# Performance work log

Measured on AMD Instinct MI355X. Metric: run time of the kernel, lower is better.

The kernel has to match this reference:

```python
import jax, jax.numpy as jnp
import numpy as np

PATCH = 16
ATT_DEPTH = 2
DOWN = 2 ** ATT_DEPTH  # 4


def _unfold(x, p):
    # torch nn.Unfold(kernel=p, stride=p) on (B, C, H, W) single-channel slices,
    # vectorized over C. Returns (B, C, p*p, L) with L = (H//p)*(W//p),
    # kernel elements in row-major order, patches in row-major order (matches torch).
    B, C, H, W = x.shape
    xr = x.reshape(B, C, H // p, p, W // p, p)
    xr = xr.transpose(0, 1, 3, 5, 2, 4)  # (B, C, p, p, H//p, W//p)
    return xr.reshape(B, C, p * p, (H // p) * (W // p))


def setup_inputs() -> dict:
    key = jax.random.key(0)
    k1, k2, k3 = jax.random.split(key, 3)
    B, C, H, W = 8, 4, 1024, 1024
    L = (H // PATCH) * (W // PATCH)            # 4096
    L2 = (H // DOWN // PATCH) * (W // DOWN // PATCH)  # 256
    pred = jax.random.normal(k1, (B, C, H, W), dtype=jnp.float32)
    target = jax.random.randint(k2, (B, H, W), 0, C, dtype=jnp.int64)
    attentions = jax.random.uniform(k3, (B, C, L, L2), dtype=jnp.float32)
    return {"pred": pred, "target": target, "attentions": attentions}


def reference(pred, target, attentions):
    B, C, H, W = pred.shape
    # activation (softmax over class dim); pred is not used further in the loss,
    # kept for faithfulness to the original forward.
    _ = jax.nn.softmax(pred, axis=1)
    # one-hot ground truth, (B, C, H, W) float32
    y_gt = (target[:, None, :, :] == jnp.arange(C, dtype=target.dtype)[None, :, None, None]).astype(jnp.float32)
    # grouped conv with all-ones 4x4 kernel, stride 4, divided by 16 == 4x4 average pool
    y_gt_conv = y_gt.reshape(B, C, H // DOWN, DOWN, W // DOWN, DOWN).mean(axis=(3, 5))
    # unfold both maps: (B, C, p*p, L) and (B, C, p*p, L2)
    u_gt = _unfold(y_gt, PATCH)
    u_conv = _unfold(y_gt_conv, PATCH)
    # att[b,c,l,m] = sum_k u_gt[b,c,k,l] * u_conv[b,c,k,m] / p^2
    attentions_gt = jnp.einsum('bckl,bckm->bclm', u_gt, u_conv) / float(PATCH * PATCH)
    # MSE (mean reduction)
    return jnp.mean((attentions - attentions_gt) ** 2)
```

## Files before the change

kernel.cpp:

```cpp
#include <hip/hip_runtime.h>
#include <stdint.h>


#define BDIM 256

typedef int v4i  __attribute__((ext_vector_type(4)));
typedef int v16i __attribute__((ext_vector_type(16)));

__global__ __launch_bounds__(BDIM) void prep_kernel(
    const int* __restrict__ tgt, uint8_t* __restrict__ cls,
    uint8_t* __restrict__ cntT, float* __restrict__ dout) {
  __shared__ uint4 lcls[16][17];
  const int t   = threadIdx.x;
  const int blk = blockIdx.x;
  if (blk == 0 && t == 0) *dout = 0.f;
  const int b  = blk >> 8;
  const int hr = (blk >> 2) & 63;
  const int wq = blk & 3;

  {
    const int row = t >> 4, wb = t & 15;
    const int* p = tgt + ((size_t)b << 20) + ((size_t)((hr << 4) + row) << 10)
                 + (wq << 8) + (wb << 4);
    uint32_t o[4];
#pragma unroll
    for (int i = 0; i < 4; ++i) {
      int4 v = *(const int4*)(p + (i << 2));
      o[i] = (uint32_t)v.x | ((uint32_t)v.y << 8) |
             ((uint32_t)v.z << 16) | ((uint32_t)v.w << 24);
    }
    lcls[row][wb] = make_uint4(o[0], o[1], o[2], o[3]);
  }
  __syncthreads();

  {
    const int wb = t >> 4, ky = t & 15;
    const int l = (hr << 6) + (wq << 4) + wb;
    *(uint4*)(cls + ((size_t)b << 20) + ((size_t)l << 8) + (ky << 4)) =
        lcls[ky][wb];
  }

  {
    const int py = t >> 6, px = t & 63;
    uint32_t pc = 0;
#pragma unroll
    for (int dy = 0; dy < 4; ++dy) {
      uint32_t wv = ((const uint32_t*)&lcls[(py << 2) + dy][px >> 2])[px & 3];
#pragma unroll
      for (int s = 0; s < 32; s += 8)
        pc += 1u << (((wv >> s) & 3u) << 3);
    }
    const int Y = (hr << 2) + py, X = (wq << 6) + px;
    const int m  = ((Y >> 4) << 4) | (X >> 4);
    const int km = ((Y & 15) << 4) | (X & 15);
    size_t o = ((size_t)b << 18) | ((size_t)m << 8) | (size_t)km;
#pragma unroll
    for (int c = 0; c < 4; ++c)
      cntT[o + ((size_t)c << 16)] = (uint8_t)((pc >> (c << 3)) & 0xFFu);
  }
}

__global__ __launch_bounds__(BDIM) void gemm_kernel(
    const uint8_t* __restrict__ cls, const uint8_t* __restrict__ cntT,
    const float* __restrict__ att, float* __restrict__ dout) {
  __shared__ float wsum[4];
  const int t    = threadIdx.x;
  const int wv   = t >> 6, lane = t & 63;
  const int bc   = blockIdx.y;
  const int b    = bc >> 2, c = bc & 3;
  const int l0   = (blockIdx.x << 7) + (wv << 5);
  const int lrow  = lane & 31;
  const int khalf = lane >> 5;

  const uint32_t crep = (uint32_t)c * 0x01010101u;
  v4i afr[8];
  const uint8_t* abase = cls + ((size_t)b << 20) +
                         ((size_t)(l0 + lrow) << 8) + (khalf << 4);
#pragma unroll
  for (int kk = 0; kk < 8; ++kk) {
    uint4 raw = *(const uint4*)(abase + (kk << 5));
    uint32_t r[4] = {raw.x, raw.y, raw.z, raw.w};
    v4i a;
#pragma unroll
    for (int i = 0; i < 4; ++i) {
      uint32_t x = r[i] ^ crep;
      uint32_t nz = (x | (x >> 1)) & 0x01010101u;
      a[i] = (int)(nz ^ 0x01010101u);
    }
    afr[kk] = a;
  }

  const uint8_t* bbase = cntT + ((size_t)bc << 16) + (khalf << 4);
  const float* attbase = att + ((size_t)bc << 20) +
                         ((size_t)(l0 + (khalf << 2)) << 8) + lrow;
  float lsum = 0.f;

#pragma unroll 1
  for (int mc = 0; mc < 8; ++mc) {
    const float* ap = attbase + (mc << 5);
    float av[16];
#pragma unroll
    for (int reg = 0; reg < 16; ++reg)
      av[reg] = ap[((reg & 3) << 8) + ((reg >> 2) << 11)];

    v16i acc = {0,0,0,0,0,0,0,0,0,0,0,0,0,0,0,0};
    const uint8_t* bb = bbase + ((size_t)((mc << 5) + lrow) << 8);
#pragma unroll
    for (int kk = 0; kk < 8; ++kk) {
      uint4 raw = *(const uint4*)(bb + (kk << 5));
      v4i bfr;
      bfr[0] = (int)raw.x; bfr[1] = (int)raw.y;
      bfr[2] = (int)raw.z; bfr[3] = (int)raw.w;
      acc = __builtin_amdgcn_mfma_i32_32x32x32_i8(afr[kk], bfr, acc, 0, 0, 0);
    }
#pragma unroll
    for (int reg = 0; reg < 16; ++reg) {
      float d = fmaf((float)acc[reg], -1.f / 4096.f, av[reg]);
      lsum = fmaf(d, d, lsum);
    }
  }

#pragma unroll
  for (int o = 32; o > 0; o >>= 1) lsum += __shfl_down(lsum, o, 64);
  if (lane == 0) wsum[wv] = lsum;
  __syncthreads();
  if (t == 0) {
    float s = (wsum[0] + wsum[1]) + (wsum[2] + wsum[3]);
    atomicAdd(dout, s * (1.f / 33554432.f));
  }
}

extern "C" void kernel_launch(void* const* d_in, const int* in_sizes, int n_in,
                              void* d_out, int out_size, void* d_ws, size_t ws_size,
                              hipStream_t stream) {
  (void)in_sizes; (void)n_in; (void)out_size; (void)ws_size;
  const int*   tgt = (const int*)d_in[1];
  const float* att = (const float*)d_in[2];
  float* dout      = (float*)d_out;
  uint8_t* cls     = (uint8_t*)d_ws;
  uint8_t* cntT    = (uint8_t*)d_ws + (8u << 20);

  prep_kernel<<<dim3(2048), BDIM, 0, stream>>>(tgt, cls, cntT, dout);
  gemm_kernel<<<dim3(32, 32), BDIM, 0, stream>>>(cls, cntT, att, dout);
}
```

Measured before the change: 279.0 us.

## Stage GEMM results in LDS and stream attentions with coalesced float4 loads

```diff
diff --git a/kernel.cpp b/kernel.cpp
--- a/kernel.cpp
+++ b/kernel.cpp
@@ -3,6 +3,7 @@
 
 
 #define BDIM 256
+#define GST 264
 
 typedef int v4i  __attribute__((ext_vector_type(4)));
 typedef int v16i __attribute__((ext_vector_type(16)));
@@ -60,22 +61,26 @@
   }
 }
 
-__global__ __launch_bounds__(BDIM) void gemm_kernel(
+__global__ __launch_bounds__(BDIM, 4) void gemm_kernel(
     const uint8_t* __restrict__ cls, const uint8_t* __restrict__ cntT,
     const float* __restrict__ att, float* __restrict__ dout) {
+  __shared__ uint16_t gt[64][GST];
   __shared__ float wsum[4];
   const int t    = threadIdx.x;
   const int wv   = t >> 6, lane = t & 63;
   const int bc   = blockIdx.y;
   const int b    = bc >> 2, c = bc & 3;
-  const int l0   = (blockIdx.x << 7) + (wv << 5);
+  const int lb   = blockIdx.x << 6;
+  const int strip = wv & 1;
+  const int mh    = wv >> 1;
   const int lrow  = lane & 31;
   const int khalf = lane >> 5;
 
   const uint32_t crep = (uint32_t)c * 0x01010101u;
   v4i afr[8];
   const uint8_t* abase = cls + ((size_t)b << 20) +
-                         ((size_t)(l0 + lrow) << 8) + (khalf << 4);
+                         ((size_t)(lb + (strip << 5) + lrow) << 8) +
+                         (khalf << 4);
 #pragma unroll
   for (int kk = 0; kk < 8; ++kk) {
     uint4 raw = *(const uint4*)(abase + (kk << 5));
@@ -91,18 +96,10 @@
   }
 
   const uint8_t* bbase = cntT + ((size_t)bc << 16) + (khalf << 4);
-  const float* attbase = att + ((size_t)bc << 20) +
-                         ((size_t)(l0 + (khalf << 2)) << 8) + lrow;
-  float lsum = 0.f;
 
 #pragma unroll 1
-  for (int mc = 0; mc < 8; ++mc) {
-    const float* ap = attbase + (mc << 5);
-    float av[16];
-#pragma unroll
-    for (int reg = 0; reg < 16; ++reg)
-      av[reg] = ap[((reg & 3) << 8) + ((reg >> 2) << 11)];
-
+  for (int i = 0; i < 4; ++i) {
+    const int mc = (mh << 2) + i;
     v16i acc = {0,0,0,0,0,0,0,0,0,0,0,0,0,0,0,0};
     const uint8_t* bb = bbase + ((size_t)((mc << 5) + lrow) << 8);
 #pragma unroll
@@ -113,11 +110,34 @@
       bfr[2] = (int)raw.z; bfr[3] = (int)raw.w;
       acc = __builtin_amdgcn_mfma_i32_32x32x32_i8(afr[kk], bfr, acc, 0, 0, 0);
     }
+    const int col = (mc << 5) + lrow;
 #pragma unroll
     for (int reg = 0; reg < 16; ++reg) {
-      float d = fmaf((float)acc[reg], -1.f / 4096.f, av[reg]);
-      lsum = fmaf(d, d, lsum);
+      const int row = (strip << 5) + (reg & 3) + ((reg >> 2) << 3) +
+                      (khalf << 2);
+      gt[row][col] = (uint16_t)acc[reg];
     }
+  }
+  __syncthreads();
+
+  const float4* ab = (const float4*)(att + ((size_t)bc << 20) +
+                                     ((size_t)lb << 8));
+  float lsum = 0.f;
+#pragma unroll 4
+  for (int it = 0; it < 16; ++it) {
+    const int idx = (it << 8) + t;
+    float4 av = ab[idx];
+    const int row = idx >> 6, c4 = (idx & 63) << 2;
+    const uint16_t* g = &gt[row][c4];
+    ushort4 gv = *(const ushort4*)g;
+    float d0 = fmaf((float)gv.x, -1.f / 4096.f, av.x);
+    float d1 = fmaf((float)gv.y, -1.f / 4096.f, av.y);
+    float d2 = fmaf((float)gv.z, -1.f / 4096.f, av.z);
+    float d3 = fmaf((float)gv.w, -1.f / 4096.f, av.w);
+    lsum = fmaf(d0, d0, lsum);
+    lsum = fmaf(d1, d1, lsum);
+    lsum = fmaf(d2, d2, lsum);
+    lsum = fmaf(d3, d3, lsum);
   }
 
 #pragma unroll
@@ -141,5 +161,5 @@
   uint8_t* cntT    = (uint8_t*)d_ws + (8u << 20);
 
   prep_kernel<<<dim3(2048), BDIM, 0, stream>>>(tgt, cls, cntT, dout);
-  gemm_kernel<<<dim3(32, 32), BDIM, 0, stream>>>(cls, cntT, att, dout);
+  gemm_kernel<<<dim3(64, 32), BDIM, 0, stream>>>(cls, cntT, att, dout);
 }
```

Measured after the change: 294.5 us. +5.5%, slower.

## Stage B counts in swizzled LDS and split M across twice as many blocks

Applied to the files above, without the earlier changes.

```diff
diff --git a/kernel.cpp b/kernel.cpp
--- a/kernel.cpp
+++ b/kernel.cpp
@@ -60,22 +60,35 @@
   }
 }
 
-__global__ __launch_bounds__(BDIM) void gemm_kernel(
+__global__ __launch_bounds__(BDIM, 4) void gemm_kernel(
     const uint8_t* __restrict__ cls, const uint8_t* __restrict__ cntT,
     const float* __restrict__ att, float* __restrict__ dout) {
+  __shared__ uint4 cB[2048];
   __shared__ float wsum[4];
   const int t    = threadIdx.x;
   const int wv   = t >> 6, lane = t & 63;
   const int bc   = blockIdx.y;
   const int b    = bc >> 2, c = bc & 3;
-  const int l0   = (blockIdx.x << 7) + (wv << 5);
+  const int lb   = (blockIdx.x >> 1) << 7;
+  const int mbase = (blockIdx.x & 1) << 7;
   const int lrow  = lane & 31;
   const int khalf = lane >> 5;
+
+  {
+    const uint4* gp = (const uint4*)(cntT + ((size_t)bc << 16) + (mbase << 8));
+#pragma unroll
+    for (int j = 0; j < 8; ++j) {
+      const int idx16 = (j << 8) + t;
+      const int mr    = idx16 >> 4;
+      const int slot  = (idx16 & 15) ^ (mr & 15);
+      cB[(mr << 4) | slot] = gp[idx16];
+    }
+  }
 
   const uint32_t crep = (uint32_t)c * 0x01010101u;
   v4i afr[8];
   const uint8_t* abase = cls + ((size_t)b << 20) +
-                         ((size_t)(l0 + lrow) << 8) + (khalf << 4);
+                         ((size_t)(lb + (wv << 5) + lrow) << 8) + (khalf << 4);
 #pragma unroll
   for (int kk = 0; kk < 8; ++kk) {
     uint4 raw = *(const uint4*)(abase + (kk << 5));
@@ -90,24 +103,27 @@
     afr[kk] = a;
   }
 
-  const uint8_t* bbase = cntT + ((size_t)bc << 16) + (khalf << 4);
+  __syncthreads();
+
   const float* attbase = att + ((size_t)bc << 20) +
-                         ((size_t)(l0 + (khalf << 2)) << 8) + lrow;
-  float lsum = 0.f;
+                         ((size_t)(lb + (wv << 5) + (khalf << 2)) << 8) +
+                         mbase + lrow;
+  float ls[4] = {0.f, 0.f, 0.f, 0.f};
 
-#pragma unroll 1
-  for (int mc = 0; mc < 8; ++mc) {
+#pragma unroll
+  for (int mc = 0; mc < 4; ++mc) {
     const float* ap = attbase + (mc << 5);
     float av[16];
 #pragma unroll
     for (int reg = 0; reg < 16; ++reg)
       av[reg] = ap[((reg & 3) << 8) + ((reg >> 2) << 11)];
 
+    const int mr = (mc << 5) + lrow;
     v16i acc = {0,0,0,0,0,0,0,0,0,0,0,0,0,0,0,0};
-    const uint8_t* bb = bbase + ((size_t)((mc << 5) + lrow) << 8);
 #pragma unroll
     for (int kk = 0; kk < 8; ++kk) {
-      uint4 raw = *(const uint4*)(bb + (kk << 5));
+      const int slot = ((kk << 1) + khalf) ^ (mr & 15);
+      uint4 raw = cB[(mr << 4) | slot];
       v4i bfr;
       bfr[0] = (int)raw.x; bfr[1] = (int)raw.y;
       bfr[2] = (int)raw.z; bfr[3] = (int)raw.w;
@@ -116,10 +132,11 @@
 #pragma unroll
     for (int reg = 0; reg < 16; ++reg) {
       float d = fmaf((float)acc[reg], -1.f / 4096.f, av[reg]);
-      lsum = fmaf(d, d, lsum);
+      ls[reg & 3] = fmaf(d, d, ls[reg & 3]);
     }
   }
 
+  float lsum = (ls[0] + ls[1]) + (ls[2] + ls[3]);
 #pragma unroll
   for (int o = 32; o > 0; o >>= 1) lsum += __shfl_down(lsum, o, 64);
   if (lane == 0) wsum[wv] = lsum;
@@ -141,5 +158,5 @@
   uint8_t* cntT    = (uint8_t*)d_ws + (8u << 20);
 
   prep_kernel<<<dim3(2048), BDIM, 0, stream>>>(tgt, cls, cntT, dout);
-  gemm_kernel<<<dim3(32, 32), BDIM, 0, stream>>>(cls, cntT, att, dout);
+  gemm_kernel<<<dim3(64, 32), BDIM, 0, stream>>>(cls, cntT, att, dout);
 }
```

Result: faster. 267.9 us (-4.0%).
